# Kernel optimization log

Measured on AMD Instinct MI355X. Metric: run time of the kernel, lower is better.

Reference implementation:

```python
import jax, jax.numpy as jnp
import numpy as np
import math

B, S, D = 16, 2048, 128

def setup_inputs() -> dict:
    key = jax.random.key(0)
    k1, k2, k3, k4 = jax.random.split(key, 4)
    query = jax.random.normal(k1, (B, S, D), dtype=jnp.float32)
    key_t = jax.random.normal(k2, (B, S, D), dtype=jnp.float32)
    value = jax.random.normal(k3, (B, S, D), dtype=jnp.float32)
    attn_mask = jax.random.randint(k4, (B, S, S), 0, 2).astype(bool)
    return {"query": query, "key": key_t, "value": value, "attn_mask": attn_mask}

def reference(query, key, value, attn_mask):
    # score = Q K^T / sqrt(d)  -> [B, Sq, Sk]
    scale = 1.0 / math.sqrt(query.shape[-1])
    score = jnp.einsum('bqd,bkd->bqk', query, key) * scale
    # faithful quirk: masked positions are replaced by the VALUE 1e-9 (not -inf)
    mask_score = jnp.where(attn_mask, jnp.float32(1e-9), score)
    # faithful quirk: softmax over dim=1 (the query axis), as in the torch source
    score_matrix = jax.nn.softmax(mask_score, axis=1)
    # output = softmax(scores) @ V  -> [B, Sq, D]
    output = jnp.einsum('bqk,bkd->bqd', score_matrix, value)
    return output
```

## Files before the change

### kernel.cpp

```cpp
#include <hip/hip_runtime.h>
#include <math.h>

#define NB 16
#define SS 2048
#define DQ 128
#define SCALE 0.08838834764831845f

typedef __bf16 bf16x8 __attribute__((ext_vector_type(8)));
typedef unsigned short ushort8_t __attribute__((ext_vector_type(8)));
typedef float floatx4 __attribute__((ext_vector_type(4)));

__device__ __forceinline__ unsigned short f2bf(float x) {
  unsigned int u = __float_as_uint(x);
  u += 0x7fffu + ((u >> 16) & 1u);
  return (unsigned short)(u >> 16);
}
union FragU { ushort8_t u; bf16x8 b; };
__device__ __forceinline__ bf16x8 ld_frag(const unsigned short* p) {
  FragU t; t.u = *(const ushort8_t*)p; return t.b;
}
__device__ __forceinline__ floatx4 mfma16(bf16x8 a, bf16x8 b, floatx4 c) {
  return __builtin_amdgcn_mfma_f32_16x16x32_bf16(a, b, c, 0, 0, 0);
}


__global__ void zero_accum(float* __restrict__ O) {
  float* p = O + (size_t)blockIdx.x * SS * DQ + 16 * DQ;
#pragma unroll
  for (int i = 0; i < 8; ++i) p[threadIdx.x + 256 * i] = 0.f;
}

__global__ __launch_bounds__(256, 4) void pass1_colsum(
    const float* __restrict__ Q, const float* __restrict__ K,
    const int* __restrict__ M, float* __restrict__ O)
{
  const int k0  = blockIdx.x * 64;
  const int b   = blockIdx.y;
  const int qc  = blockIdx.z;
  const int tid = threadIdx.x;
  const int w = tid >> 6, lane = tid & 63, l15 = lane & 15, quad = lane >> 4;

  __shared__ unsigned short Kbf[64][136];
  __shared__ unsigned short Qbf[64][136];
  __shared__ float red[4][64];

  const float* Qb = Q + (size_t)b * SS * DQ;
  const float* Kb = K + (size_t)b * SS * DQ;
  const int*   Mb = M + (size_t)b * SS * SS;

#pragma unroll
  for (int r = 0; r < 8; ++r) {
    int idx = tid + r * 256;
    int row = idx >> 5, c4 = (idx & 31) * 4;
    float4 v = *(const float4*)(Kb + (size_t)(k0 + row) * DQ + c4);
    *(ushort4*)&Kbf[row][c4] = make_ushort4(f2bf(v.x), f2bf(v.y), f2bf(v.z), f2bf(v.w));
  }

  float colacc[16];
#pragma unroll
  for (int t = 0; t < 16; ++t) colacc[t] = 0.f;

  const int qlane = 16 * w + l15;

  for (int qi = 0; qi < 8; ++qi) {
    const int q0 = qc * 512 + qi * 64;
    __syncthreads();
#pragma unroll
    for (int r = 0; r < 8; ++r) {
      int idx = tid + r * 256;
      int row = idx >> 5, c4 = (idx & 31) * 4;
      float4 v = *(const float4*)(Qb + (size_t)(q0 + row) * DQ + c4);
      *(ushort4*)&Qbf[row][c4] = make_ushort4(f2bf(v.x), f2bf(v.y), f2bf(v.z), f2bf(v.w));
    }
    int4 mv[4];
#pragma unroll
    for (int i = 0; i < 4; ++i)
      mv[i] = *(const int4*)(Mb + (size_t)(q0 + qlane) * SS + k0 + 16 * i + quad * 4);
    __syncthreads();

    floatx4 acc[4];
#pragma unroll
    for (int i = 0; i < 4; ++i) acc[i] = (floatx4){0.f, 0.f, 0.f, 0.f};
#pragma unroll
    for (int d0 = 0; d0 < DQ; d0 += 32) {
      bf16x8 bq = ld_frag(&Qbf[qlane][d0 + quad * 8]);
#pragma unroll
      for (int i = 0; i < 4; ++i) {
        bf16x8 ak = ld_frag(&Kbf[16 * i + l15][d0 + quad * 8]);
        acc[i] = mfma16(ak, bq, acc[i]);
      }
    }
#pragma unroll
    for (int i = 0; i < 4; ++i) {
      int mm[4] = {mv[i].x, mv[i].y, mv[i].z, mv[i].w};
#pragma unroll
      for (int r = 0; r < 4; ++r) {
        float s = mm[r] ? 1e-9f : acc[i][r] * SCALE;
        colacc[i * 4 + r] += __expf(s);
      }
    }
  }

#pragma unroll
  for (int t = 0; t < 16; ++t) {
    colacc[t] += __shfl_xor(colacc[t], 1, 64);
    colacc[t] += __shfl_xor(colacc[t], 2, 64);
    colacc[t] += __shfl_xor(colacc[t], 4, 64);
    colacc[t] += __shfl_xor(colacc[t], 8, 64);
  }
  if (l15 == 0) {
#pragma unroll
    for (int i = 0; i < 4; ++i)
#pragma unroll
      for (int r = 0; r < 4; ++r)
        red[w][16 * i + quad * 4 + r] = colacc[i * 4 + r];
  }
  __syncthreads();
  if (tid < 64) {
    float s = red[0][tid] + red[1][tid] + red[2][tid] + red[3][tid];
    atomicAdd(O + (size_t)b * SS * DQ + 16 * DQ + k0 + tid, s);
  }
}

__global__ void combine_linv(float* __restrict__ O) {
  const int b  = blockIdx.x;
  const int jb = blockIdx.y * 4;
  float* Ob = O + (size_t)b * SS * DQ;
#pragma unroll
  for (int it = 0; it < 8; ++it) {
    int k = threadIdx.x + 256 * it;
    float inv = 1.0f / Ob[16 * DQ + k];
#pragma unroll
    for (int j = 0; j < 4; ++j)
      Ob[(size_t)(64 * (jb + j)) * DQ + k] = inv;
  }
}

__global__ __launch_bounds__(256, 3) void pass2_out(
    const float* __restrict__ Q, const float* __restrict__ K,
    const float* __restrict__ V, const int* __restrict__ M,
    float* __restrict__ O)
{
  const int b = blockIdx.y, q0 = blockIdx.x * 64;
  const int tid = threadIdx.x;
  const int w = tid >> 6, lane = tid & 63, l15 = lane & 15, quad = lane >> 4;

  __shared__ unsigned short Kbf[64][136];
  __shared__ unsigned short Es[64][72];
  __shared__ unsigned short Wt[128][72];
  __shared__ float Li[SS];

  const float* Qb = Q + (size_t)b * SS * DQ;
  const float* Kb = K + (size_t)b * SS * DQ;
  const float* Vb = V + (size_t)b * SS * DQ;
  const int*   Mb = M + (size_t)b * SS * SS;

  {
    const float* src = O + ((size_t)b * SS + q0) * DQ;
#pragma unroll
    for (int r = 0; r < 2; ++r) {
      int idx = (tid + r * 256) * 4;
      *(float4*)&Li[idx] = *(const float4*)(src + idx);
    }
  }
  FragU qf[4];
  {
    const float* qrow = Qb + (size_t)(q0 + 16 * w + l15) * DQ;
#pragma unroll
    for (int i = 0; i < 4; ++i) {
      float4 a = *(const float4*)(qrow + 32 * i + quad * 8);
      float4 c = *(const float4*)(qrow + 32 * i + quad * 8 + 4);
      qf[i].u = (ushort8_t){f2bf(a.x), f2bf(a.y), f2bf(a.z), f2bf(a.w),
                            f2bf(c.x), f2bf(c.y), f2bf(c.z), f2bf(c.w)};
    }
  }

  floatx4 accO[8];
#pragma unroll
  for (int j = 0; j < 8; ++j) accO[j] = (floatx4){0.f, 0.f, 0.f, 0.f};

  const int* mrow = Mb + (size_t)(q0 + 16 * w + l15) * SS;

  for (int k0 = 0; k0 < SS; k0 += 64) {
    __syncthreads();

#pragma unroll
    for (int r = 0; r < 8; ++r) {
      int idx = tid + r * 256;
      int row = idx >> 5, c4 = (idx & 31) * 4;
      float4 v = *(const float4*)(Kb + (size_t)(k0 + row) * DQ + c4);
      *(ushort4*)&Kbf[row][c4] = make_ushort4(f2bf(v.x), f2bf(v.y), f2bf(v.z), f2bf(v.w));
    }
#pragma unroll
    for (int r = 0; r < 4; ++r) {
      int idx = tid + r * 256;
      int k2  = (idx >> 5) * 2;
      int c4  = (idx & 31) * 4;
      float4 va = *(const float4*)(Vb + (size_t)(k0 + k2) * DQ + c4);
      float4 vb = *(const float4*)(Vb + (size_t)(k0 + k2 + 1) * DQ + c4);
      float fa[4] = {va.x, va.y, va.z, va.w};
      float fb[4] = {vb.x, vb.y, vb.z, vb.w};
#pragma unroll
      for (int i = 0; i < 4; ++i) {
        int d  = c4 + i;
        int kk = k2 ^ ((((unsigned)d >> 2) & 7) << 3);
        *(ushort2*)&Wt[d][kk] = make_ushort2(f2bf(fa[i]), f2bf(fb[i]));
      }
    }
    int4 mv[4];
#pragma unroll
    for (int j = 0; j < 4; ++j)
      mv[j] = *(const int4*)(mrow + k0 + 16 * j + quad * 4);
    __syncthreads();

    floatx4 acc[4];
#pragma unroll
    for (int j = 0; j < 4; ++j) acc[j] = (floatx4){0.f, 0.f, 0.f, 0.f};
#pragma unroll
    for (int i = 0; i < 4; ++i) {
      bf16x8 bq = qf[i].b;
#pragma unroll
      for (int j = 0; j < 4; ++j) {
        bf16x8 ak = ld_frag(&Kbf[16 * j + l15][32 * i + quad * 8]);
        acc[j] = mfma16(ak, bq, acc[j]);
      }
    }
#pragma unroll
    for (int j = 0; j < 4; ++j) {
      float4 liv = *(const float4*)&Li[k0 + 16 * j + quad * 4];
      float lv[4] = {liv.x, liv.y, liv.z, liv.w};
      int mm[4] = {mv[j].x, mv[j].y, mv[j].z, mv[j].w};
      unsigned short es[4];
#pragma unroll
      for (int r = 0; r < 4; ++r) {
        float s = mm[r] ? 1e-9f : acc[j][r] * SCALE;
        es[r] = f2bf(__expf(s) * lv[r]);
      }
      *(ushort4*)&Es[16 * w + l15][16 * j + quad * 4] =
          make_ushort4(es[0], es[1], es[2], es[3]);
    }
#pragma unroll
    for (int c = 0; c < 2; ++c) {
      bf16x8 be = ld_frag(&Es[16 * w + l15][32 * c + quad * 8]);
#pragma unroll
      for (int j = 0; j < 8; ++j) {
        int d  = 16 * j + l15;
        int kk = (32 * c + quad * 8) ^ ((((unsigned)d >> 2) & 7) << 3);
        bf16x8 aw = ld_frag(&Wt[d][kk]);
        accO[j] = mfma16(aw, be, accO[j]);
      }
    }
  }

#pragma unroll
  for (int j = 0; j < 8; ++j) {
    float* op = O + ((size_t)b * SS + q0 + 16 * w + l15) * DQ + 16 * j + quad * 4;
    *(float4*)op = make_float4(accO[j][0], accO[j][1], accO[j][2], accO[j][3]);
  }
}

extern "C" void kernel_launch(void* const* d_in, const int* in_sizes, int n_in,
                              void* d_out, int out_size, void* d_ws, size_t ws_size,
                              hipStream_t stream) {
  const float* Q = (const float*)d_in[0];
  const float* K = (const float*)d_in[1];
  const float* V = (const float*)d_in[2];
  const int*   M = (const int*)d_in[3];
  float* O = (float*)d_out;
  (void)d_ws; (void)ws_size;

  zero_accum<<<dim3(NB), 256, 0, stream>>>(O);
  pass1_colsum<<<dim3(32, NB, 4), 256, 0, stream>>>(Q, K, M, O);
  combine_linv<<<dim3(NB, 8), 256, 0, stream>>>(O);
  pass2_out<<<dim3(32, NB), 256, 0, stream>>>(Q, K, V, M, O);
}
```

Before: 576.8 us.

## Register-prefetch next Q/K/V/mask tiles and use LDS-only barriers

Both passes now load the next iteration's global tiles (Q and mask in pass 1; K, V and mask in pass 2) into registers right after the barrier, so the loads overlap with the current tile's MFMA and softmax work. __syncthreads is replaced by an s_waitcnt lgkmcnt(0) + s_barrier that does not wait on outstanding global loads. pass2 launch bounds drop from 3 to 2 waves per SIMD to leave room for the extra prefetch registers. This costs occupancy in pass2 in exchange for hiding global memory latency.

```diff
diff --git a/kernel.cpp b/kernel.cpp
--- a/kernel.cpp
+++ b/kernel.cpp
@@ -21,6 +21,10 @@
 }
 __device__ __forceinline__ floatx4 mfma16(bf16x8 a, bf16x8 b, floatx4 c) {
   return __builtin_amdgcn_mfma_f32_16x16x32_bf16(a, b, c, 0, 0, 0);
+}
+
+__device__ __forceinline__ void bar_lds() {
+  asm volatile("s_waitcnt lgkmcnt(0)\n\ts_barrier" ::: "memory");
 }
 
 
@@ -48,35 +52,53 @@
   const float* Kb = K + (size_t)b * SS * DQ;
   const int*   Mb = M + (size_t)b * SS * SS;
 
+  const int srow = tid >> 5;
+  const int sc4  = (tid & 31) * 4;
+
 #pragma unroll
   for (int r = 0; r < 8; ++r) {
-    int idx = tid + r * 256;
-    int row = idx >> 5, c4 = (idx & 31) * 4;
-    float4 v = *(const float4*)(Kb + (size_t)(k0 + row) * DQ + c4);
-    *(ushort4*)&Kbf[row][c4] = make_ushort4(f2bf(v.x), f2bf(v.y), f2bf(v.z), f2bf(v.w));
+    int row = srow + r * 8;
+    float4 v = *(const float4*)(Kb + (size_t)(k0 + row) * DQ + sc4);
+    *(ushort4*)&Kbf[row][sc4] = make_ushort4(f2bf(v.x), f2bf(v.y), f2bf(v.z), f2bf(v.w));
+  }
+
+  const int qlane = 16 * w + l15;
+
+  float4 qreg[8];
+  int4 mv_nxt[4];
+  {
+    const int q0 = qc * 512;
+#pragma unroll
+    for (int r = 0; r < 8; ++r)
+      qreg[r] = *(const float4*)(Qb + (size_t)(q0 + srow + r * 8) * DQ + sc4);
+#pragma unroll
+    for (int i = 0; i < 4; ++i)
+      mv_nxt[i] = *(const int4*)(Mb + (size_t)(q0 + qlane) * SS + k0 + 16 * i + quad * 4);
   }
 
   float colacc[16];
 #pragma unroll
   for (int t = 0; t < 16; ++t) colacc[t] = 0.f;
 
-  const int qlane = 16 * w + l15;
-
   for (int qi = 0; qi < 8; ++qi) {
-    const int q0 = qc * 512 + qi * 64;
-    __syncthreads();
+    bar_lds();
+    int4 mv[4] = {mv_nxt[0], mv_nxt[1], mv_nxt[2], mv_nxt[3]};
 #pragma unroll
     for (int r = 0; r < 8; ++r) {
-      int idx = tid + r * 256;
-      int row = idx >> 5, c4 = (idx & 31) * 4;
-      float4 v = *(const float4*)(Qb + (size_t)(q0 + row) * DQ + c4);
-      *(ushort4*)&Qbf[row][c4] = make_ushort4(f2bf(v.x), f2bf(v.y), f2bf(v.z), f2bf(v.w));
-    }
-    int4 mv[4];
-#pragma unroll
-    for (int i = 0; i < 4; ++i)
-      mv[i] = *(const int4*)(Mb + (size_t)(q0 + qlane) * SS + k0 + 16 * i + quad * 4);
-    __syncthreads();
+      float4 v = qreg[r];
+      *(ushort4*)&Qbf[srow + r * 8][sc4] =
+          make_ushort4(f2bf(v.x), f2bf(v.y), f2bf(v.z), f2bf(v.w));
+    }
+    bar_lds();
+    if (qi < 7) {
+      const int qn = qc * 512 + (qi + 1) * 64;
+#pragma unroll
+      for (int r = 0; r < 8; ++r)
+        qreg[r] = *(const float4*)(Qb + (size_t)(qn + srow + r * 8) * DQ + sc4);
+#pragma unroll
+      for (int i = 0; i < 4; ++i)
+        mv_nxt[i] = *(const int4*)(Mb + (size_t)(qn + qlane) * SS + k0 + 16 * i + quad * 4);
+    }
 
     floatx4 acc[4];
 #pragma unroll
@@ -115,7 +137,7 @@
       for (int r = 0; r < 4; ++r)
         red[w][16 * i + quad * 4 + r] = colacc[i * 4 + r];
   }
-  __syncthreads();
+  bar_lds();
   if (tid < 64) {
     float s = red[0][tid] + red[1][tid] + red[2][tid] + red[3][tid];
     atomicAdd(O + (size_t)b * SS * DQ + 16 * DQ + k0 + tid, s);
@@ -136,7 +158,7 @@
   }
 }
 
-__global__ __launch_bounds__(256, 3) void pass2_out(
+__global__ __launch_bounds__(256, 2) void pass2_out(
     const float* __restrict__ Q, const float* __restrict__ K,
     const float* __restrict__ V, const int* __restrict__ M,
     float* __restrict__ O)
@@ -155,6 +177,9 @@
   const float* Vb = V + (size_t)b * SS * DQ;
   const int*   Mb = M + (size_t)b * SS * SS;
 
+  const int srow = tid >> 5;
+  const int sc4  = (tid & 31) * 4;
+
   {
     const float* src = O + ((size_t)b * SS + q0) * DQ;
 #pragma unroll
@@ -181,37 +206,63 @@
 
   const int* mrow = Mb + (size_t)(q0 + 16 * w + l15) * SS;
 
+  float4 kreg[8], vreg[8];
+  int4 mv_nxt[4];
+  const int vk2 = (tid >> 5) * 2;
+  {
+#pragma unroll
+    for (int r = 0; r < 8; ++r)
+      kreg[r] = *(const float4*)(Kb + (size_t)(srow + r * 8) * DQ + sc4);
+#pragma unroll
+    for (int r = 0; r < 4; ++r) {
+      int k2 = vk2 + r * 16;
+      vreg[2 * r]     = *(const float4*)(Vb + (size_t)(k2)     * DQ + sc4);
+      vreg[2 * r + 1] = *(const float4*)(Vb + (size_t)(k2 + 1) * DQ + sc4);
+    }
+#pragma unroll
+    for (int j = 0; j < 4; ++j)
+      mv_nxt[j] = *(const int4*)(mrow + 16 * j + quad * 4);
+  }
+
   for (int k0 = 0; k0 < SS; k0 += 64) {
-    __syncthreads();
+    bar_lds();
+    int4 mv[4] = {mv_nxt[0], mv_nxt[1], mv_nxt[2], mv_nxt[3]};
 
 #pragma unroll
     for (int r = 0; r < 8; ++r) {
-      int idx = tid + r * 256;
-      int row = idx >> 5, c4 = (idx & 31) * 4;
-      float4 v = *(const float4*)(Kb + (size_t)(k0 + row) * DQ + c4);
-      *(ushort4*)&Kbf[row][c4] = make_ushort4(f2bf(v.x), f2bf(v.y), f2bf(v.z), f2bf(v.w));
+      float4 v = kreg[r];
+      *(ushort4*)&Kbf[srow + r * 8][sc4] =
+          make_ushort4(f2bf(v.x), f2bf(v.y), f2bf(v.z), f2bf(v.w));
     }
 #pragma unroll
     for (int r = 0; r < 4; ++r) {
-      int idx = tid + r * 256;
-      int k2  = (idx >> 5) * 2;
-      int c4  = (idx & 31) * 4;
-      float4 va = *(const float4*)(Vb + (size_t)(k0 + k2) * DQ + c4);
-      float4 vb = *(const float4*)(Vb + (size_t)(k0 + k2 + 1) * DQ + c4);
-      float fa[4] = {va.x, va.y, va.z, va.w};
-      float fb[4] = {vb.x, vb.y, vb.z, vb.w};
+      int k2 = vk2 + r * 16;
+      float fa[4] = {vreg[2*r].x, vreg[2*r].y, vreg[2*r].z, vreg[2*r].w};
+      float fb[4] = {vreg[2*r+1].x, vreg[2*r+1].y, vreg[2*r+1].z, vreg[2*r+1].w};
 #pragma unroll
       for (int i = 0; i < 4; ++i) {
-        int d  = c4 + i;
+        int d  = sc4 + i;
         int kk = k2 ^ ((((unsigned)d >> 2) & 7) << 3);
         *(ushort2*)&Wt[d][kk] = make_ushort2(f2bf(fa[i]), f2bf(fb[i]));
       }
     }
-    int4 mv[4];
-#pragma unroll
-    for (int j = 0; j < 4; ++j)
-      mv[j] = *(const int4*)(mrow + k0 + 16 * j + quad * 4);
-    __syncthreads();
+    bar_lds();
+
+    if (k0 + 64 < SS) {
+      const int kn = k0 + 64;
+#pragma unroll
+      for (int r = 0; r < 8; ++r)
+        kreg[r] = *(const float4*)(Kb + (size_t)(kn + srow + r * 8) * DQ + sc4);
+#pragma unroll
+      for (int r = 0; r < 4; ++r) {
+        int k2 = vk2 + r * 16;
+        vreg[2 * r]     = *(const float4*)(Vb + (size_t)(kn + k2)     * DQ + sc4);
+        vreg[2 * r + 1] = *(const float4*)(Vb + (size_t)(kn + k2 + 1) * DQ + sc4);
+      }
+#pragma unroll
+      for (int j = 0; j < 4; ++j)
+        mv_nxt[j] = *(const int4*)(mrow + kn + 16 * j + quad * 4);
+    }
 
     floatx4 acc[4];
 #pragma unroll
```

Result: faster. 517.8 us (-10.2%).
